# Kernel optimization log

Measured on AMD Instinct MI355X. Metric: run time of the kernel, lower is better.

The kernel has to match this reference:

```python
import jax, jax.numpy as jnp
import numpy as np

EPS = 1e-8
LAM = 0.7  # resonance_lambda


def phase_resonance(a, b, eps=EPS):
    # a, b: (B, N, D) float32. Pairwise phase coherence -> (B, N, N)
    D = a.shape[-1]
    pairs = (D // 2)
    a2 = a[..., :pairs * 2].reshape(*a.shape[:-1], pairs, 2)
    b2 = b[..., :pairs * 2].reshape(*b.shape[:-1], pairs, 2)
    theta_a = jnp.arctan2(a2[..., 1] + eps, a2[..., 0] + eps)  # (B,N,pairs)
    theta_b = jnp.arctan2(b2[..., 1] + eps, b2[..., 0] + eps)  # (B,N,pairs)
    delta = theta_a[:, :, None, :] - theta_b[:, None, :, :]    # (B,N,N,pairs)
    return jnp.cos(delta).mean(axis=-1)                        # (B,N,N)


def setup_inputs() -> dict:
    key = jax.random.key(0)
    k1, k2, k3, k4, k5 = jax.random.split(key, 5)
    B, N, D = 2, 1024, 128
    node_states = jax.random.normal(k1, (B, N, D), dtype=jnp.float32)
    node_gates = jax.random.uniform(k2, (B, N, 1), dtype=jnp.float32)
    r_acc = jax.random.normal(k3, (B, N, N), dtype=jnp.float32)
    # nn.Linear(D, D, bias=False) weights, y = x @ W.T
    scale = 1.0 / np.sqrt(D)
    W_in = jax.random.uniform(k4, (D, D), dtype=jnp.float32, minval=-scale, maxval=scale)
    W_out = jax.random.uniform(k5, (D, D), dtype=jnp.float32, minval=-scale, maxval=scale)
    conductance = jnp.asarray(1.0, dtype=jnp.float32)
    return {"node_states": node_states, "node_gates": node_gates, "r_acc": r_acc,
            "W_in": W_in, "W_out": W_out, "conductance": conductance}


def reference(node_states, node_gates, r_acc, W_in, W_out, conductance):
    B, N, D = node_states.shape
    h = node_states @ W_in.T                                   # field_in projection
    r_instant = phase_resonance(h, h)                          # (B,N,N)
    r_acc_new = LAM * r_acc + (1.0 - LAM) * r_instant
    r_acc_new = jnp.clip(r_acc_new, -2.0, 2.0)
    cond = jnp.clip(conductance, -5.0, 5.0)
    coupling = jax.nn.sigmoid(cond * r_acc_new)                # (B,N,N)
    eye = jnp.eye(N, dtype=coupling.dtype)[None]               # zero self-coupling
    coupling = coupling * (1.0 - eye)
    coupling = coupling * jnp.swapaxes(node_gates, -1, -2)     # (B,1,N) col gates
    coupling = coupling * node_gates                           # (B,N,1) row gates
    coupling = coupling / (coupling.sum(axis=-1, keepdims=True) + 1e-8)
    transmitted = node_states * node_gates
    values = transmitted @ W_out.T                             # field_out projection
    field_signal = coupling @ values                           # (B,N,D)
    return field_signal, r_acc_new
```

## Files before the change

### kernel.cpp

```cpp
#include <hip/hip_runtime.h>
#include <hip/hip_bf16.h>

using bf16x8 = __attribute__((ext_vector_type(8))) short;
using bf16x4 = __attribute__((ext_vector_type(4))) short;
using f32x4  = __attribute__((ext_vector_type(4))) float;

#define NN 1024
#define DD 128

__device__ __forceinline__ short bf16bits(float f) {
    __hip_bfloat16 t = __float2bfloat16(f);
    return *(short*)&t;
}

__global__ __launch_bounds__(256) void prep_kernel(
    const float* __restrict__ states, const float* __restrict__ gates,
    const float* __restrict__ W_in, const float* __restrict__ W_out,
    __hip_bfloat16* __restrict__ M_bf, __hip_bfloat16* __restrict__ valT)
{
    __shared__ float s_state[4 * 128];
    __shared__ float s_WinT[32 * 129];
    __shared__ float s_WoutT[32 * 129];
    __shared__ float s_v[4][128];
    __shared__ float s_g[4];

    const int tid = threadIdx.x;
    const int b  = blockIdx.x >> 8;
    const int n0 = (blockIdx.x & 255) * 4;

    const float* sb = states + ((size_t)b * NN + n0) * DD;
    if (tid < 128) ((float4*)s_state)[tid] = ((const float4*)sb)[tid];
    if (tid < 4)   s_g[tid] = gates[b * NN + n0 + tid];

    const int c  = tid & 127;
    const int rg = tid >> 7;
    float acc_h[2] = {0.f, 0.f};
    float acc_v[2] = {0.f, 0.f};

    const int kq = tid & 7;
    const int dl = tid >> 3;
    for (int k0 = 0; k0 < 128; k0 += 32) {
        __syncthreads();
        #pragma unroll
        for (int dp = 0; dp < 4; ++dp) {
            int d = dp * 32 + dl;
            float4 w1 = *(const float4*)(W_in  + d * 128 + k0 + kq * 4);
            float4 w2 = *(const float4*)(W_out + d * 128 + k0 + kq * 4);
            s_WinT [(kq * 4 + 0) * 129 + d] = w1.x;
            s_WinT [(kq * 4 + 1) * 129 + d] = w1.y;
            s_WinT [(kq * 4 + 2) * 129 + d] = w1.z;
            s_WinT [(kq * 4 + 3) * 129 + d] = w1.w;
            s_WoutT[(kq * 4 + 0) * 129 + d] = w2.x;
            s_WoutT[(kq * 4 + 1) * 129 + d] = w2.y;
            s_WoutT[(kq * 4 + 2) * 129 + d] = w2.z;
            s_WoutT[(kq * 4 + 3) * 129 + d] = w2.w;
        }
        __syncthreads();
        #pragma unroll
        for (int k2 = 0; k2 < 32; ++k2) {
            float w1 = s_WinT [k2 * 129 + c];
            float w2 = s_WoutT[k2 * 129 + c];
            #pragma unroll
            for (int r = 0; r < 2; ++r) {
                float s = s_state[(rg * 2 + r) * 128 + k0 + k2];
                acc_h[r] = fmaf(s, w1, acc_h[r]);
                acc_v[r] = fmaf(s, w2, acc_v[r]);
            }
        }
    }

    #pragma unroll
    for (int r = 0; r < 2; ++r) {
        int row = rg * 2 + r;
        float hm = acc_h[r] + 1e-8f;
        float hp = __shfl_xor(hm, 1);
        float x = (c & 1) ? hp : hm;
        float y = (c & 1) ? hm : hp;
        float r2 = x * x + y * y;
        float out;
        if (r2 > 0.f) out = ((c & 1) ? y : x) * rsqrtf(r2);
        else          out = (c & 1) ? 0.f : 1.f;
        M_bf[((size_t)b * NN + n0 + row) * DD + c] = __float2bfloat16(out);
        s_v[row][c] = acc_v[r] * s_g[row];
    }
    __syncthreads();

    if (tid < 128) {
        bf16x4 pk;
        #pragma unroll
        for (int r = 0; r < 4; ++r) pk[r] = bf16bits(s_v[r][tid]);
        *(bf16x4*)(valT + ((size_t)b * DD + tid) * NN + n0) = pk;
    }
}

__global__ __launch_bounds__(256) void fused_kernel(
    const __hip_bfloat16* __restrict__ M_bf,
    const __hip_bfloat16* __restrict__ valT,
    const float* __restrict__ r_acc,
    const float* __restrict__ gates,
    const float* __restrict__ cond_ptr,
    float* __restrict__ r_out,
    __hip_bfloat16* __restrict__ part,
    float* __restrict__ part_rs)
{
    __shared__ __align__(16) __hip_bfloat16 s_cpl[2][16][72];
    __shared__ float s_rs[32][2];

    const int tid = threadIdx.x;
    const int l  = tid & 63;
    const int w  = tid >> 6;
    const int wi = w & 1;
    const int wj = w >> 1;
    const int row_a = l & 15;
    const int kg    = l >> 4;

    const int jt = blockIdx.x;
    const int j0 = jt * 64;
    const int i0 = blockIdx.y * 32;
    const int b  = blockIdx.z;

    const bf16x8* Mv = (const bf16x8*)(M_bf + (size_t)b * NN * DD);
    const bf16x8* Vv = (const bf16x8*)(valT + (size_t)b * DD * NN);

    f32x4 acc[2];
    acc[0] = (f32x4){0.f, 0.f, 0.f, 0.f};
    acc[1] = (f32x4){0.f, 0.f, 0.f, 0.f};
    #pragma unroll
    for (int ks = 0; ks < 4; ++ks) {
        int kv = ks * 4 + kg;
        bf16x8 a = Mv[(size_t)(i0 + wi * 16 + row_a) * 16 + kv];
        #pragma unroll
        for (int cp = 0; cp < 2; ++cp) {
            bf16x8 bb = Mv[(size_t)(j0 + wj * 32 + cp * 16 + row_a) * 16 + kv];
            acc[cp] = __builtin_amdgcn_mfma_f32_16x16x32_bf16(a, bb, acc[cp], 0, 0, 0);
        }
    }

    float cond = fminf(fmaxf(cond_ptr[0], -5.f), 5.f);
    const int i_base = i0 + wi * 16 + kg * 4;

    float g_j[2], g_i[4];
    #pragma unroll
    for (int cp = 0; cp < 2; ++cp) g_j[cp] = gates[b * NN + j0 + wj * 32 + cp * 16 + row_a];
    #pragma unroll
    for (int q = 0; q < 4; ++q)    g_i[q]  = gates[b * NN + i_base + q];

    const size_t robase = (size_t)b * NN * NN;
    float rs[4] = {0.f, 0.f, 0.f, 0.f};

    #pragma unroll
    for (int q = 0; q < 4; ++q) {
        int i = i_base + q;
        float gi = g_i[q];
        #pragma unroll
        for (int cp = 0; cp < 2; ++cp) {
            int jl = wj * 32 + cp * 16 + row_a;
            int j  = j0 + jl;
            float s  = acc[cp][q] * (1.f / 64.f);
            float ra = r_acc[robase + (size_t)i * NN + j];
            float rn = fminf(fmaxf(0.7f * ra + 0.3f * s, -2.f), 2.f);
            r_out[robase + (size_t)i * NN + j] = rn;
            float cpl = (i == j) ? 0.f
                        : (1.f / (1.f + __expf(-cond * rn))) * gi * g_j[cp];
            rs[q] += cpl;
            s_cpl[wi][kg * 4 + q][jl] = __float2bfloat16(cpl);
        }
    }

    #pragma unroll
    for (int q = 0; q < 4; ++q) {
        float v = rs[q];
        v += __shfl_xor(v, 1);
        v += __shfl_xor(v, 2);
        v += __shfl_xor(v, 4);
        v += __shfl_xor(v, 8);
        if (row_a == 0) s_rs[wi * 16 + kg * 4 + q][wj] = v;
    }
    __syncthreads();

    f32x4 pacc[4];
    #pragma unroll
    for (int dt = 0; dt < 4; ++dt) pacc[dt] = (f32x4){0.f, 0.f, 0.f, 0.f};

    #pragma unroll
    for (int ks2 = 0; ks2 < 2; ++ks2) {
        bf16x8 a = *(const bf16x8*)&s_cpl[wi][row_a][ks2 * 32 + kg * 8];
        #pragma unroll
        for (int dt = 0; dt < 4; ++dt) {
            int d = (wj * 4 + dt) * 16 + row_a;
            bf16x8 bb = Vv[(size_t)d * (NN / 8) + (j0 >> 3) + ks2 * 4 + kg];
            pacc[dt] = __builtin_amdgcn_mfma_f32_16x16x32_bf16(a, bb, pacc[dt], 0, 0, 0);
        }
    }

    __hip_bfloat16* pb = part + ((size_t)jt * 2 + b) * NN * DD;
    #pragma unroll
    for (int dt = 0; dt < 4; ++dt) {
        #pragma unroll
        for (int q = 0; q < 4; ++q) {
            int i = i0 + wi * 16 + kg * 4 + q;
            int d = (wj * 4 + dt) * 16 + row_a;
            pb[(size_t)i * DD + d] = __float2bfloat16(pacc[dt][q]);
        }
    }

    if (tid < 32)
        part_rs[((size_t)jt * 2 + b) * NN + i0 + tid] = s_rs[tid][0] + s_rs[tid][1];
}

__global__ __launch_bounds__(256) void reduce_kernel(
    const __hip_bfloat16* __restrict__ part,
    const float* __restrict__ part_rs,
    float* __restrict__ field)
{
    int t   = blockIdx.x * 256 + threadIdx.x;
    int b   = t >> 15;
    int rem = t & 32767;
    int i   = rem >> 5;
    int d4  = (rem & 31) * 4;
    size_t ibase = (size_t)i * DD + d4;

    float s0 = 0.f, s1 = 0.f, s2 = 0.f, s3 = 0.f, rsum = 0.f;
    #pragma unroll
    for (int jt = 0; jt < 16; ++jt) {
        size_t slab = ((size_t)jt * 2 + b);
        uint2 u = *(const uint2*)(part + slab * NN * DD + ibase);
        s0 += __uint_as_float(u.x << 16);
        s1 += __uint_as_float(u.x & 0xffff0000u);
        s2 += __uint_as_float(u.y << 16);
        s3 += __uint_as_float(u.y & 0xffff0000u);
        rsum += part_rs[slab * NN + i];
    }
    float inv = 1.0f / (rsum + 1e-8f);
    float4 o = {s0 * inv, s1 * inv, s2 * inv, s3 * inv};
    *(float4*)(field + ((size_t)b * NN + i) * DD + d4) = o;
}

extern "C" void kernel_launch(void* const* d_in, const int* in_sizes, int n_in,
                              void* d_out, int out_size, void* d_ws, size_t ws_size,
                              hipStream_t stream) {
    const float* states = (const float*)d_in[0];
    const float* gates  = (const float*)d_in[1];
    const float* r_acc  = (const float*)d_in[2];
    const float* W_in   = (const float*)d_in[3];
    const float* W_out  = (const float*)d_in[4];
    const float* cond   = (const float*)d_in[5];

    float* field = (float*)d_out;
    float* r_out = field + 2 * NN * DD;

    char* ws = (char*)d_ws;
    __hip_bfloat16* M_bf    = (__hip_bfloat16*)ws;
    __hip_bfloat16* valT    = (__hip_bfloat16*)(ws + (512 << 10));
    __hip_bfloat16* part    = (__hip_bfloat16*)(ws + (1 << 20));
    float*          part_rs = (float*)(ws + (9 << 20));

    hipLaunchKernelGGL(prep_kernel, dim3(512), dim3(256), 0, stream,
                       states, gates, W_in, W_out, M_bf, valT);
    hipLaunchKernelGGL(fused_kernel, dim3(16, 32, 2), dim3(256), 0, stream,
                       M_bf, valT, r_acc, gates, cond, r_out, part, part_rs);
    hipLaunchKernelGGL(reduce_kernel, dim3(256), dim3(256), 0, stream,
                       part, part_rs, field);
}
```

Before: 101.1 us.

## Use MFMA bf16 for input projections and widen fused j-tile to 128

The prep kernel's scalar FP32 projection with LDS-transposed weights is replaced by bf16 MFMA tiles over 16 rows per block, converting inputs on the fly and staging outputs in shared memory for vectorized stores. The fused kernel's j-tile doubles from 64 to 128 columns, halving the number of partial slabs that must be written and then summed in the reduce kernel. This lowers partial-sum traffic and prep compute at the cost of rounding the projection inputs to bf16, and it launches fewer blocks.

```diff
diff --git a/kernel.cpp b/kernel.cpp
--- a/kernel.cpp
+++ b/kernel.cpp
@@ -2,15 +2,23 @@
 #include <hip/hip_bf16.h>
 
 using bf16x8 = __attribute__((ext_vector_type(8))) short;
-using bf16x4 = __attribute__((ext_vector_type(4))) short;
 using f32x4  = __attribute__((ext_vector_type(4))) float;
 
 #define NN 1024
 #define DD 128
 
-__device__ __forceinline__ short bf16bits(float f) {
+__device__ __forceinline__ short bf16b(float f) {
     __hip_bfloat16 t = __float2bfloat16(f);
     return *(short*)&t;
+}
+
+__device__ __forceinline__ bf16x8 cvt8(const float* __restrict__ p) {
+    float4 a = *(const float4*)p;
+    float4 b = *(const float4*)(p + 4);
+    bf16x8 r;
+    r[0] = bf16b(a.x); r[1] = bf16b(a.y); r[2] = bf16b(a.z); r[3] = bf16b(a.w);
+    r[4] = bf16b(b.x); r[5] = bf16b(b.y); r[6] = bf16b(b.z); r[7] = bf16b(b.w);
+    return r;
 }
 
 __global__ __launch_bounds__(256) void prep_kernel(
@@ -18,78 +26,71 @@
     const float* __restrict__ W_in, const float* __restrict__ W_out,
     __hip_bfloat16* __restrict__ M_bf, __hip_bfloat16* __restrict__ valT)
 {
-    __shared__ float s_state[4 * 128];
-    __shared__ float s_WinT[32 * 129];
-    __shared__ float s_WoutT[32 * 129];
-    __shared__ float s_v[4][128];
-    __shared__ float s_g[4];
+    __shared__ __align__(16) short s_m[16][136];
+    __shared__ __align__(16) short s_vT[128][24];
 
     const int tid = threadIdx.x;
-    const int b  = blockIdx.x >> 8;
-    const int n0 = (blockIdx.x & 255) * 4;
-
-    const float* sb = states + ((size_t)b * NN + n0) * DD;
-    if (tid < 128) ((float4*)s_state)[tid] = ((const float4*)sb)[tid];
-    if (tid < 4)   s_g[tid] = gates[b * NN + n0 + tid];
-
-    const int c  = tid & 127;
-    const int rg = tid >> 7;
-    float acc_h[2] = {0.f, 0.f};
-    float acc_v[2] = {0.f, 0.f};
-
-    const int kq = tid & 7;
-    const int dl = tid >> 3;
-    for (int k0 = 0; k0 < 128; k0 += 32) {
-        __syncthreads();
-        #pragma unroll
-        for (int dp = 0; dp < 4; ++dp) {
-            int d = dp * 32 + dl;
-            float4 w1 = *(const float4*)(W_in  + d * 128 + k0 + kq * 4);
-            float4 w2 = *(const float4*)(W_out + d * 128 + k0 + kq * 4);
-            s_WinT [(kq * 4 + 0) * 129 + d] = w1.x;
-            s_WinT [(kq * 4 + 1) * 129 + d] = w1.y;
-            s_WinT [(kq * 4 + 2) * 129 + d] = w1.z;
-            s_WinT [(kq * 4 + 3) * 129 + d] = w1.w;
-            s_WoutT[(kq * 4 + 0) * 129 + d] = w2.x;
-            s_WoutT[(kq * 4 + 1) * 129 + d] = w2.y;
-            s_WoutT[(kq * 4 + 2) * 129 + d] = w2.z;
-            s_WoutT[(kq * 4 + 3) * 129 + d] = w2.w;
-        }
-        __syncthreads();
-        #pragma unroll
-        for (int k2 = 0; k2 < 32; ++k2) {
-            float w1 = s_WinT [k2 * 129 + c];
-            float w2 = s_WoutT[k2 * 129 + c];
-            #pragma unroll
-            for (int r = 0; r < 2; ++r) {
-                float s = s_state[(rg * 2 + r) * 128 + k0 + k2];
-                acc_h[r] = fmaf(s, w1, acc_h[r]);
-                acc_v[r] = fmaf(s, w2, acc_v[r]);
-            }
-        }
-    }
-
-    #pragma unroll
-    for (int r = 0; r < 2; ++r) {
-        int row = rg * 2 + r;
-        float hm = acc_h[r] + 1e-8f;
-        float hp = __shfl_xor(hm, 1);
-        float x = (c & 1) ? hp : hm;
-        float y = (c & 1) ? hm : hp;
-        float r2 = x * x + y * y;
-        float out;
-        if (r2 > 0.f) out = ((c & 1) ? y : x) * rsqrtf(r2);
-        else          out = (c & 1) ? 0.f : 1.f;
-        M_bf[((size_t)b * NN + n0 + row) * DD + c] = __float2bfloat16(out);
-        s_v[row][c] = acc_v[r] * s_g[row];
+    const int l = tid & 63, w = tid >> 6;
+    const int row_a = l & 15, kg = l >> 4;
+    const int b  = blockIdx.x >> 6;
+    const int n0 = (blockIdx.x & 63) * 16;
+    const int colbase = w * 32;
+
+    const float* A = states + ((size_t)b * NN + n0) * DD;
+
+    f32x4 accH[2], accV[2];
+    #pragma unroll
+    for (int cp = 0; cp < 2; ++cp) {
+        accH[cp] = (f32x4){0.f, 0.f, 0.f, 0.f};
+        accV[cp] = (f32x4){0.f, 0.f, 0.f, 0.f};
+    }
+
+    #pragma unroll
+    for (int ks = 0; ks < 4; ++ks) {
+        int koff = (ks * 4 + kg) * 8;
+        bf16x8 a = cvt8(A + row_a * DD + koff);
+        #pragma unroll
+        for (int cp = 0; cp < 2; ++cp) {
+            int d = colbase + cp * 16 + row_a;
+            bf16x8 b1 = cvt8(W_in  + d * DD + koff);
+            bf16x8 b2 = cvt8(W_out + d * DD + koff);
+            accH[cp] = __builtin_amdgcn_mfma_f32_16x16x32_bf16(a, b1, accH[cp], 0, 0, 0);
+            accV[cp] = __builtin_amdgcn_mfma_f32_16x16x32_bf16(a, b2, accV[cp], 0, 0, 0);
+        }
+    }
+
+    float g[4];
+    #pragma unroll
+    for (int q = 0; q < 4; ++q) g[q] = gates[b * NN + n0 + kg * 4 + q];
+
+    const bool odd = (row_a & 1) != 0;
+    #pragma unroll
+    for (int cp = 0; cp < 2; ++cp) {
+        #pragma unroll
+        for (int q = 0; q < 4; ++q) {
+            float hm = accH[cp][q] + 1e-8f;
+            float hp = __shfl_xor(hm, 1);
+            float x = odd ? hp : hm;
+            float y = odd ? hm : hp;
+            float r2 = x * x + y * y;
+            float out;
+            if (r2 > 0.f) out = (odd ? y : x) * rsqrtf(r2);
+            else          out = odd ? 0.f : 1.f;
+            s_m[kg * 4 + q][colbase + cp * 16 + row_a] = bf16b(out);
+            s_vT[colbase + cp * 16 + row_a][kg * 4 + q] = bf16b(accV[cp][q] * g[q]);
+        }
     }
     __syncthreads();
 
-    if (tid < 128) {
-        bf16x4 pk;
-        #pragma unroll
-        for (int r = 0; r < 4; ++r) pk[r] = bf16bits(s_v[r][tid]);
-        *(bf16x4*)(valT + ((size_t)b * DD + tid) * NN + n0) = pk;
+    {
+        int r = tid >> 4, seg = tid & 15;
+        bf16x8 v = *(const bf16x8*)&s_m[r][seg * 8];
+        *(bf16x8*)(M_bf + ((size_t)b * NN + n0 + r) * DD + seg * 8) = v;
+    }
+    {
+        int d = tid >> 1, half = tid & 1;
+        bf16x8 v = *(const bf16x8*)&s_vT[d][half * 8];
+        *(bf16x8*)(valT + ((size_t)b * DD + d) * NN + n0 + half * 8) = v;
     }
 }
 
@@ -103,7 +104,7 @@
     __hip_bfloat16* __restrict__ part,
     float* __restrict__ part_rs)
 {
-    __shared__ __align__(16) __hip_bfloat16 s_cpl[2][16][72];
+    __shared__ __align__(16) short s_cpl[2][16][136];
     __shared__ float s_rs[32][2];
 
     const int tid = threadIdx.x;
@@ -115,23 +116,24 @@
     const int kg    = l >> 4;
 
     const int jt = blockIdx.x;
-    const int j0 = jt * 64;
+    const int j0 = jt * 128;
     const int i0 = blockIdx.y * 32;
     const int b  = blockIdx.z;
 
     const bf16x8* Mv = (const bf16x8*)(M_bf + (size_t)b * NN * DD);
     const bf16x8* Vv = (const bf16x8*)(valT + (size_t)b * DD * NN);
 
-    f32x4 acc[2];
-    acc[0] = (f32x4){0.f, 0.f, 0.f, 0.f};
-    acc[1] = (f32x4){0.f, 0.f, 0.f, 0.f};
+    f32x4 acc[4];
+    #pragma unroll
+    for (int cp = 0; cp < 4; ++cp) acc[cp] = (f32x4){0.f, 0.f, 0.f, 0.f};
+
     #pragma unroll
     for (int ks = 0; ks < 4; ++ks) {
         int kv = ks * 4 + kg;
         bf16x8 a = Mv[(size_t)(i0 + wi * 16 + row_a) * 16 + kv];
         #pragma unroll
-        for (int cp = 0; cp < 2; ++cp) {
-            bf16x8 bb = Mv[(size_t)(j0 + wj * 32 + cp * 16 + row_a) * 16 + kv];
+        for (int cp = 0; cp < 4; ++cp) {
+            bf16x8 bb = Mv[(size_t)(j0 + wj * 64 + cp * 16 + row_a) * 16 + kv];
             acc[cp] = __builtin_amdgcn_mfma_f32_16x16x32_bf16(a, bb, acc[cp], 0, 0, 0);
         }
     }
@@ -139,9 +141,9 @@
     float cond = fminf(fmaxf(cond_ptr[0], -5.f), 5.f);
     const int i_base = i0 + wi * 16 + kg * 4;
 
-    float g_j[2], g_i[4];
-    #pragma unroll
-    for (int cp = 0; cp < 2; ++cp) g_j[cp] = gates[b * NN + j0 + wj * 32 + cp * 16 + row_a];
+    float g_j[4], g_i[4];
+    #pragma unroll
+    for (int cp = 0; cp < 4; ++cp) g_j[cp] = gates[b * NN + j0 + wj * 64 + cp * 16 + row_a];
     #pragma unroll
     for (int q = 0; q < 4; ++q)    g_i[q]  = gates[b * NN + i_base + q];
 
@@ -153,8 +155,8 @@
         int i = i_base + q;
         float gi = g_i[q];
         #pragma unroll
-        for (int cp = 0; cp < 2; ++cp) {
-            int jl = wj * 32 + cp * 16 + row_a;
+        for (int cp = 0; cp < 4; ++cp) {
+            int jl = wj * 64 + cp * 16 + row_a;
             int j  = j0 + jl;
             float s  = acc[cp][q] * (1.f / 64.f);
             float ra = r_acc[robase + (size_t)i * NN + j];
@@ -163,7 +165,7 @@
             float cpl = (i == j) ? 0.f
                         : (1.f / (1.f + __expf(-cond * rn))) * gi * g_j[cp];
             rs[q] += cpl;
-            s_cpl[wi][kg * 4 + q][jl] = __float2bfloat16(cpl);
+            s_cpl[wi][kg * 4 + q][jl] = bf16b(cpl);
         }
     }
 
@@ -183,11 +185,11 @@
     for (int dt = 0; dt < 4; ++dt) pacc[dt] = (f32x4){0.f, 0.f, 0.f, 0.f};
 
     #pragma unroll
-    for (int ks2 = 0; ks2 < 2; ++ks2) {
-        bf16x8 a = *(const bf16x8*)&s_cpl[wi][row_a][ks2 * 32 + kg * 8];
+    for (int ks2 = 0; ks2 < 4; ++ks2) {
+        bf16x8 a = *(const bf16x8*)&s_cpl[wi][row_a][(ks2 * 4 + kg) * 8];
         #pragma unroll
         for (int dt = 0; dt < 4; ++dt) {
-            int d = (wj * 4 + dt) * 16 + row_a;
+            int d = wj * 64 + dt * 16 + row_a;
             bf16x8 bb = Vv[(size_t)d * (NN / 8) + (j0 >> 3) + ks2 * 4 + kg];
             pacc[dt] = __builtin_amdgcn_mfma_f32_16x16x32_bf16(a, bb, pacc[dt], 0, 0, 0);
         }
@@ -199,7 +201,7 @@
         #pragma unroll
         for (int q = 0; q < 4; ++q) {
             int i = i0 + wi * 16 + kg * 4 + q;
-            int d = (wj * 4 + dt) * 16 + row_a;
+            int d = wj * 64 + dt * 16 + row_a;
             pb[(size_t)i * DD + d] = __float2bfloat16(pacc[dt][q]);
         }
     }
@@ -222,7 +224,7 @@
 
     float s0 = 0.f, s1 = 0.f, s2 = 0.f, s3 = 0.f, rsum = 0.f;
     #pragma unroll
-    for (int jt = 0; jt < 16; ++jt) {
+    for (int jt = 0; jt < 8; ++jt) {
         size_t slab = ((size_t)jt * 2 + b);
         uint2 u = *(const uint2*)(part + slab * NN * DD + ibase);
         s0 += __uint_as_float(u.x << 16);
@@ -253,11 +255,11 @@
     __hip_bfloat16* M_bf    = (__hip_bfloat16*)ws;
     __hip_bfloat16* valT    = (__hip_bfloat16*)(ws + (512 << 10));
     __hip_bfloat16* part    = (__hip_bfloat16*)(ws + (1 << 20));
-    float*          part_rs = (float*)(ws + (9 << 20));
-
-    hipLaunchKernelGGL(prep_kernel, dim3(512), dim3(256), 0, stream,
+    float*          part_rs = (float*)(ws + (5 << 20));
+
+    hipLaunchKernelGGL(prep_kernel, dim3(128), dim3(256), 0, stream,
                        states, gates, W_in, W_out, M_bf, valT);
-    hipLaunchKernelGGL(fused_kernel, dim3(16, 32, 2), dim3(256), 0, stream,
+    hipLaunchKernelGGL(fused_kernel, dim3(8, 32, 2), dim3(256), 0, stream,
                        M_bf, valT, r_acc, gates, cond, r_out, part, part_rs);
     hipLaunchKernelGGL(reduce_kernel, dim3(256), dim3(256), 0, stream,
                        part, part_rs, field);
```

Result: faster. 98.08 us (-3.0%).
